# Kernel optimization log

Measured on AMD Instinct MI355X. Metric: run time of the kernel, lower is better.

Reference implementation:

```python
import jax, jax.numpy as jnp
import numpy as np
import math

B, S, E = 16, 600, 300   # batch, seq_len, enc_len
H, NC = 512, 2           # hidden, classes
D = S * E                # archi[0] = 180000


def setup_inputs() -> dict:
    key = jax.random.key(0)
    ks = jax.random.split(key, 7)
    x = jax.random.normal(ks[0], (B, S, E), dtype=jnp.float32)
    y = jax.random.randint(ks[1], (B,), 0, NC)
    # neurons initialized to zeros (init_neurons)
    n0 = jnp.zeros((B, S, E), jnp.float32)
    n1 = jnp.zeros((B, H), jnp.float32)
    n2 = jnp.zeros((B, NC), jnp.float32)
    # Linear weights (torch layout: [out, in]), Kaiming-uniform-like scale 1/sqrt(fan_in)
    W0 = jax.random.uniform(ks[2], (E, E), jnp.float32, -1.0, 1.0) / math.sqrt(E)
    W1 = jax.random.uniform(ks[3], (H, D), jnp.float32, -1.0, 1.0) / math.sqrt(D)
    b1 = jax.random.uniform(ks[4], (H,), jnp.float32, -1.0, 1.0) / math.sqrt(D)
    W2 = jax.random.uniform(ks[5], (NC, H), jnp.float32, -1.0, 1.0) / math.sqrt(H)
    b2 = jax.random.uniform(ks[6], (NC,), jnp.float32, -1.0, 1.0) / math.sqrt(H)
    return dict(x=x, y=y, n0=n0, n1=n1, n2=n2, W0=W0, W1=W1, b1=b1, W2=W2, b2=b2, T=3)


def reference(x, y, n0, n1, n2, W0, W1, b1, W2, b2, T):
    # EqProp free-phase relaxation (beta = 0.0, forward default).
    # Analytic dPhi/dneurons replaces torch.autograd.grad:
    scale = 1.0 / math.sqrt(E)
    Wx = jnp.einsum('bse,fe->bsf', x, W0)  # synapses[0](x), constant across steps
    for _ in range(T):
        g0 = Wx + (n1 @ W1).reshape(B, S, E)              # dPhi/dn0
        g1 = n0.reshape(B, D) @ W1.T + b1 + n2 @ W2       # dPhi/dn1
        g2 = n1 @ W2.T + b2                               # dPhi/dn2 (beta=0)
        # hand-coded attention update for neuron 0: Q=g0, K=V=x
        attn = jax.nn.softmax(scale * jnp.einsum('bse,bte->bst', g0, x), axis=-1)
        n0 = jnp.einsum('bst,bte->bse', attn, x)
        n1 = jnp.tanh(g1)
        n2 = jnp.tanh(g2)
    return n0, n1, n2
```

## Files before the change

kernel.cpp:

```cpp
#include <hip/hip_runtime.h>
#include <math.h>

#define DD 180000L
#define HH 512
#define BB 16
#define SS 600
#define EE 300
#define SP 608
#define EP 320

typedef unsigned short u16;
typedef __attribute__((ext_vector_type(8))) __bf16 bf16x8;
typedef __attribute__((ext_vector_type(4))) float f32x4;

__device__ __forceinline__ u16 f2bf(float f) {
  union { float f; unsigned int u; } x; x.f = f;
  unsigned int r = (x.u + 0x7FFFu + ((x.u >> 16) & 1u)) >> 16;
  return (u16)r;
}

__global__ __launch_bounds__(256) void k_conv_x(const float* __restrict__ x,
                                                u16* __restrict__ xb, u16* __restrict__ xt) {
  __shared__ u16 tl[32][33];
  int b = blockIdx.z;
  int tt = blockIdx.x * 32, ee = blockIdx.y * 32;
  int lx = threadIdx.x & 31, ly = threadIdx.x >> 5;
#pragma unroll
  for (int i = 0; i < 4; ++i) {
    int t = tt + ly + i * 8, e = ee + lx;
    float v = (t < SS && e < EE) ? x[((long)b * SS + t) * EE + e] : 0.f;
    u16 h = f2bf(v);
    xb[((long)b * SP + t) * EP + e] = h;
    tl[ly + i * 8][lx] = h;
  }
  __syncthreads();
#pragma unroll
  for (int i = 0; i < 4; ++i) {
    int e = ee + ly + i * 8, t = tt + lx;
    xt[((long)b * EP + e) * SP + t] = tl[lx][ly + i * 8];
  }
}

__global__ __launch_bounds__(256) void k_conv_w0(const float* __restrict__ W0, u16* __restrict__ w0b) {
  int idx = blockIdx.x * 256 + threadIdx.x;
  int f = idx / EP, e = idx % EP;
  float v = (f < EE && e < EE) ? W0[f * EE + e] : 0.f;
  w0b[idx] = f2bf(v);
}

__global__ __launch_bounds__(256) void k_gemm_nt(
    const u16* __restrict__ A, int lda, long sA, int Arows,
    const u16* __restrict__ B, int ldb, long sB, int Brows,
    float* __restrict__ C, int ldc, long sC, int Mv, int Nv, int K,
    u16* __restrict__ Cb, int ldcb, long sCb) {
  int bz = blockIdx.z;
  int m0 = blockIdx.x * 64, n0 = blockIdx.y * 64;
  int lane = threadIdx.x & 63, wv = threadIdx.x >> 6;
  int wm = m0 + (wv >> 1) * 32, wn = n0 + (wv & 1) * 32;
  int q = lane >> 4, ln = lane & 15;
  const u16* Ab = A + (long)bz * sA;
  const u16* Bb = B + (long)bz * sB;
  long arow0 = (long)min(wm + ln, Arows - 1) * lda;
  long arow1 = (long)min(wm + 16 + ln, Arows - 1) * lda;
  long brow0 = (long)min(wn + ln, Brows - 1) * ldb;
  long brow1 = (long)min(wn + 16 + ln, Brows - 1) * ldb;
  f32x4 acc00 = {0.f,0.f,0.f,0.f}, acc01 = acc00, acc10 = acc00, acc11 = acc00;
  int ksteps = (K + 31) >> 5;
  for (int kk = 0; kk < ksteps; ++kk) {
    int k0 = kk * 32 + q * 8;
    bf16x8 a0 = *(const bf16x8*)(Ab + arow0 + k0);
    bf16x8 a1 = *(const bf16x8*)(Ab + arow1 + k0);
    bf16x8 b0 = *(const bf16x8*)(Bb + brow0 + k0);
    bf16x8 bv1 = *(const bf16x8*)(Bb + brow1 + k0);
    acc00 = __builtin_amdgcn_mfma_f32_16x16x32_bf16(a0, b0,  acc00, 0, 0, 0);
    acc01 = __builtin_amdgcn_mfma_f32_16x16x32_bf16(a0, bv1, acc01, 0, 0, 0);
    acc10 = __builtin_amdgcn_mfma_f32_16x16x32_bf16(a1, b0,  acc10, 0, 0, 0);
    acc11 = __builtin_amdgcn_mfma_f32_16x16x32_bf16(a1, bv1, acc11, 0, 0, 0);
  }
  float* Cp = C + (long)bz * sC;
  u16* Cbp = Cb ? (Cb + (long)bz * sCb) : (u16*)0;
#pragma unroll
  for (int sm = 0; sm < 2; ++sm) {
#pragma unroll
    for (int sn = 0; sn < 2; ++sn) {
      f32x4 acc = (sm == 0) ? ((sn == 0) ? acc00 : acc01) : ((sn == 0) ? acc10 : acc11);
#pragma unroll
      for (int r = 0; r < 4; ++r) {
        int m = wm + sm * 16 + q * 4 + r;
        int n = wn + sn * 16 + ln;
        if (m < Mv && n < Nv) {
          float v = acc[r];
          Cp[(long)m * ldc + n] = v;
          if (Cbp) Cbp[(long)m * ldcb + n] = f2bf(v);
        }
      }
    }
  }
}

#define BN 256
#define BK 64
#define NCH 704

__global__ __launch_bounds__(256) void k_fused_w1(
    const float* __restrict__ W1, const float* __restrict__ n1f,
    const float* __restrict__ n0f, const float* __restrict__ Wx,
    u16* __restrict__ g0b, float* __restrict__ part) {
  __shared__ u16 wt[BK][BN + 8];
  __shared__ u16 n1s[BB][HH + 8];
  __shared__ u16 n0s[BB][BN + 8];
  int tid = threadIdx.x;
  long d0 = (long)blockIdx.x * BN;
#pragma unroll
  for (int i = 0; i < 8; ++i) {
    int f = i * 256 + tid;
    int b = f >> 7, c = (f & 127) * 4;
    float4 v = *(const float4*)(n1f + b * HH + c);
    n1s[b][c] = f2bf(v.x); n1s[b][c + 1] = f2bf(v.y);
    n1s[b][c + 2] = f2bf(v.z); n1s[b][c + 3] = f2bf(v.w);
  }
#pragma unroll
  for (int i = 0; i < 4; ++i) {
    int f = i * 256 + tid;
    int b = f >> 6, c = (f & 63) * 4;
    long d = d0 + c;
    float4 v = {0.f,0.f,0.f,0.f};
    if (d < DD) v = *(const float4*)(n0f + (long)b * DD + d);
    n0s[b][c] = f2bf(v.x); n0s[b][c + 1] = f2bf(v.y);
    n0s[b][c + 2] = f2bf(v.z); n0s[b][c + 3] = f2bf(v.w);
  }
  int lane = tid & 63, wv = tid >> 6, q = lane >> 4, ln = lane & 15;
  f32x4 acc0[4] = {{0.f,0.f,0.f,0.f},{0.f,0.f,0.f,0.f},{0.f,0.f,0.f,0.f},{0.f,0.f,0.f,0.f}};
  for (int s = 0; s < 8; ++s) {
    int h0 = s * BK;
    __syncthreads();
#pragma unroll
    for (int i = 0; i < 16; ++i) {
      int f = i * 256 + tid;
      int r = f >> 6, c = (f & 63) * 4;
      long d = d0 + c;
      float4 v = {0.f,0.f,0.f,0.f};
      if (d < DD) v = *(const float4*)(W1 + (long)(h0 + r) * DD + d);
      wt[r][c] = f2bf(v.x); wt[r][c + 1] = f2bf(v.y);
      wt[r][c + 2] = f2bf(v.z); wt[r][c + 3] = f2bf(v.w);
    }
    __syncthreads();
#pragma unroll
    for (int kst = 0; kst < 2; ++kst) {
      bf16x8 af = *(const bf16x8*)(&n1s[ln][h0 + kst * 32 + q * 8]);
#pragma unroll
      for (int nt = 0; nt < 4; ++nt) {
        int dc = wv * 64 + nt * 16 + ln;
        bf16x8 bv;
#pragma unroll
        for (int j = 0; j < 8; ++j) bv[j] = *(const __bf16*)(&wt[kst * 32 + q * 8 + j][dc]);
        acc0[nt] = __builtin_amdgcn_mfma_f32_16x16x32_bf16(af, bv, acc0[nt], 0, 0, 0);
      }
    }
    f32x4 acc1 = {0.f,0.f,0.f,0.f};
#pragma unroll
    for (int kst = 0; kst < 8; ++kst) {
      bf16x8 af = *(const bf16x8*)(&n0s[ln][kst * 32 + q * 8]);
      bf16x8 bv = *(const bf16x8*)(&wt[wv * 16 + ln][kst * 32 + q * 8]);
      acc1 = __builtin_amdgcn_mfma_f32_16x16x32_bf16(af, bv, acc1, 0, 0, 0);
    }
    long pb = (long)blockIdx.x * 8192;
#pragma unroll
    for (int r = 0; r < 4; ++r) {
      int b = q * 4 + r, h = h0 + wv * 16 + ln;
      part[pb + b * HH + h] = acc1[r];
    }
  }
#pragma unroll
  for (int nt = 0; nt < 4; ++nt) {
#pragma unroll
    for (int r = 0; r < 4; ++r) {
      int b = q * 4 + r;
      long d = d0 + wv * 64 + nt * 16 + ln;
      if (d < DD) {
        float val = Wx[(long)b * DD + d] + acc0[nt][r];
        int sI = (int)(d / EE), e = (int)(d % EE);
        g0b[((long)b * SS + sI) * EP + e] = f2bf(val);
      }
    }
  }
}

__global__ __launch_bounds__(256) void k_softmax(const float* __restrict__ S,
                                                 u16* __restrict__ P, float scale) {
  int s = blockIdx.x, b = blockIdx.y;
  const float* row = S + ((long)b * SP + s) * SP;
  u16* prow = P + ((long)b * SP + s) * SP;
  int tid = threadIdx.x, lane = tid & 63, wv = tid >> 6;
  __shared__ float red[8];
  float v[3]; float mx = -1e30f;
#pragma unroll
  for (int i = 0; i < 3; ++i) {
    int c = tid + i * 256;
    v[i] = (c < SS) ? row[c] * scale : -1e30f;
    mx = fmaxf(mx, v[i]);
  }
  for (int off = 32; off; off >>= 1) mx = fmaxf(mx, __shfl_down(mx, off));
  if (lane == 0) red[wv] = mx;
  __syncthreads();
  mx = fmaxf(fmaxf(red[0], red[1]), fmaxf(red[2], red[3]));
  float e[3], sum = 0.f;
#pragma unroll
  for (int i = 0; i < 3; ++i) {
    int c = tid + i * 256;
    e[i] = (c < SS) ? __expf(v[i] - mx) : 0.f;
    sum += e[i];
  }
  for (int off = 32; off; off >>= 1) sum += __shfl_down(sum, off);
  if (lane == 0) red[4 + wv] = sum;
  __syncthreads();
  float inv = 1.f / (red[4] + red[5] + red[6] + red[7]);
#pragma unroll
  for (int i = 0; i < 3; ++i) {
    int c = tid + i * 256;
    if (c < SS) prow[c] = f2bf(e[i] * inv);
  }
}

__global__ __launch_bounds__(256) void k_init(const float* __restrict__ b1, const float* __restrict__ b2,
                                              float* __restrict__ n1, float* __restrict__ n2) {
  int idx = blockIdx.x * 256 + threadIdx.x;
  n1[idx] = tanhf(b1[idx & 511]);
  if (idx < 32) n2[idx] = tanhf(b2[idx & 1]);
}

__global__ __launch_bounds__(64) void k_g2(const float* __restrict__ n1old, const float* __restrict__ W2,
                                           const float* __restrict__ b2, float* __restrict__ n2out) {
  int b = blockIdx.x >> 1, c = blockIdx.x & 1, lane = threadIdx.x;
  float s = 0.f;
#pragma unroll
  for (int i = 0; i < 8; ++i) { int h = lane + i * 64; s += n1old[b * HH + h] * W2[c * HH + h]; }
  for (int off = 32; off; off >>= 1) s += __shfl_down(s, off);
  if (lane == 0) n2out[b * 2 + c] = tanhf(s + b2[c]);
}

__global__ __launch_bounds__(256) void k_reduce1(const float* __restrict__ part, float* __restrict__ part2) {
  int idx = blockIdx.x * 256 + threadIdx.x;
  int sl = blockIdx.y;
  float s = 0.f;
  int c0 = sl * 88;
#pragma unroll 4
  for (int c = 0; c < 88; ++c) s += part[(long)(c0 + c) * 8192 + idx];
  part2[(long)sl * 8192 + idx] = s;
}

__global__ __launch_bounds__(256) void k_reduce2(const float* __restrict__ part2, const float* __restrict__ b1,
                                                 const float* __restrict__ W2, const float* __restrict__ n2old,
                                                 float* __restrict__ n1out) {
  int idx = blockIdx.x * 256 + threadIdx.x;
  int b = idx >> 9, h = idx & 511;
  float s = b1[h] + n2old[b * 2] * W2[h] + n2old[b * 2 + 1] * W2[HH + h];
#pragma unroll
  for (int sl = 0; sl < 8; ++sl) s += part2[(long)sl * 8192 + idx];
  n1out[idx] = tanhf(s);
}

extern "C" void kernel_launch(void* const* d_in, const int* in_sizes, int n_in,
                              void* d_out, int out_size, void* d_ws, size_t ws_size,
                              hipStream_t stream) {
  const float* x  = (const float*)d_in[0];
  const float* W0 = (const float*)d_in[5];
  const float* W1 = (const float*)d_in[6];
  const float* b1 = (const float*)d_in[7];
  const float* W2 = (const float*)d_in[8];
  const float* b2 = (const float*)d_in[9];

  float* out_n0 = (float*)d_out;
  float* out_n1 = out_n0 + 16L * SS * EE;
  float* out_n2 = out_n1 + 16L * HH;

  char* w = (char*)d_ws;
  auto take = [&](size_t bytes) { char* p = w; w += (bytes + 255) & ~(size_t)255; return p; };
  u16*   xb    = (u16*)take(16L * SP * EP * 2);
  u16*   xt    = (u16*)take(16L * EP * SP * 2);
  u16*   w0b   = (u16*)take((size_t)EP * EP * 2);
  float* Wx    = (float*)take(16L * SS * EE * 4);
  u16*   g0b   = (u16*)take(16L * SS * EP * 2);
  float* Sb    = (float*)take(16L * SP * SP * 4);
  u16*   attn  = (u16*)take(16L * SP * SP * 2);
  float* part2 = (float*)take(8L * 8192 * 4);
  float* n1A   = (float*)take(8192 * 4);
  float* n1B   = (float*)take(8192 * 4);
  float* n2A   = (float*)take(256);
  float* n2B   = (float*)take(256);
  float* part  = Sb;

  const float scale = 1.0f / sqrtf((float)EE);

  k_conv_x<<<dim3(19, 10, 16), 256, 0, stream>>>(x, xb, xt);
  k_conv_w0<<<400, 256, 0, stream>>>(W0, w0b);
  k_gemm_nt<<<dim3(10, 5, 16), 256, 0, stream>>>(xb, EP, (long)SP * EP, SP,
                                                 w0b, EP, 0, EP,
                                                 Wx, EE, (long)SS * EE, SS, EE, EE,
                                                 g0b, EP, (long)SS * EP);
  k_init<<<32, 256, 0, stream>>>(b1, b2, n1A, n2A);

  for (int it = 0; it < 3; ++it) {
    if (it > 0) {
      const float* n1old = (it == 1) ? n1A : n1B;
      const float* n2old = (it == 1) ? n2A : n2B;
      float* n2new = (it == 1) ? n2B : out_n2;
      float* n1new = (it == 1) ? n1B : out_n1;
      k_g2<<<32, 64, 0, stream>>>(n1old, W2, b2, n2new);
      k_fused_w1<<<NCH, 256, 0, stream>>>(W1, n1old, out_n0, Wx, g0b, part);
      k_reduce1<<<dim3(32, 8), 256, 0, stream>>>(part, part2);
      k_reduce2<<<32, 256, 0, stream>>>(part2, b1, W2, n2old, n1new);
    }
    k_gemm_nt<<<dim3(10, 10, 16), 256, 0, stream>>>(g0b, EP, (long)SS * EP, SS,
                                                    xb, EP, (long)SP * EP, SP,
                                                    Sb, SP, (long)SP * SP, SP, SP, EE,
                                                    (u16*)0, 0, 0);
    k_softmax<<<dim3(SS, 16), 256, 0, stream>>>(Sb, attn, scale);
    k_gemm_nt<<<dim3(10, 5, 16), 256, 0, stream>>>(attn, SP, (long)SP * SP, SP,
                                                   xt, SP, (long)EP * SP, EP,
                                                   out_n0, EE, (long)DD, SS, EE, SP,
                                                   (u16*)0, 0, 0);
  }
}
```

Before: 971.7 us.

## Fuse QK^T, softmax and PV into single flash-style attention kernel

Replaces the three-kernel attention path (score GEMM to fp32 buffer, softmax to bf16 buffer, PV GEMM) with one kernel per 16-row query tile. Each single-wave block holds the whole score row in registers, does the softmax in place, stages P in swizzled LDS, and multiplies by V^T directly. This removes the round trips through the large score and probability buffers and two launches. In exchange it uses very many registers per wave (38 score tiles plus 19 accumulators), runs only 608 one-wave blocks, and re-reads K and V from global memory in every block with no LDS sharing, which may limit occupancy and bandwidth. The part buffer is now allocated separately instead of aliasing the removed score buffer.

```diff
diff --git a/kernel.cpp b/kernel.cpp
--- a/kernel.cpp
+++ b/kernel.cpp
@@ -186,39 +186,105 @@
   }
 }
 
-__global__ __launch_bounds__(256) void k_softmax(const float* __restrict__ S,
-                                                 u16* __restrict__ P, float scale) {
-  int s = blockIdx.x, b = blockIdx.y;
-  const float* row = S + ((long)b * SP + s) * SP;
-  u16* prow = P + ((long)b * SP + s) * SP;
-  int tid = threadIdx.x, lane = tid & 63, wv = tid >> 6;
-  __shared__ float red[8];
-  float v[3]; float mx = -1e30f;
-#pragma unroll
-  for (int i = 0; i < 3; ++i) {
-    int c = tid + i * 256;
-    v[i] = (c < SS) ? row[c] * scale : -1e30f;
-    mx = fmaxf(mx, v[i]);
-  }
-  for (int off = 32; off; off >>= 1) mx = fmaxf(mx, __shfl_down(mx, off));
-  if (lane == 0) red[wv] = mx;
-  __syncthreads();
-  mx = fmaxf(fmaxf(red[0], red[1]), fmaxf(red[2], red[3]));
-  float e[3], sum = 0.f;
-#pragma unroll
-  for (int i = 0; i < 3; ++i) {
-    int c = tid + i * 256;
-    e[i] = (c < SS) ? __expf(v[i] - mx) : 0.f;
-    sum += e[i];
-  }
-  for (int off = 32; off; off >>= 1) sum += __shfl_down(sum, off);
-  if (lane == 0) red[4 + wv] = sum;
-  __syncthreads();
-  float inv = 1.f / (red[4] + red[5] + red[6] + red[7]);
-#pragma unroll
-  for (int i = 0; i < 3; ++i) {
-    int c = tid + i * 256;
-    if (c < SS) prow[c] = f2bf(e[i] * inv);
+#define SWZB(r) ((((r) >> 1) & 7) << 4)
+
+__global__ __launch_bounds__(64, 2) void k_attn(
+    const u16* __restrict__ Qg, const u16* __restrict__ Kg,
+    const u16* __restrict__ Vtg, float* __restrict__ O, float scale) {
+  __shared__ u16 P[16 * SP];
+  int b = blockIdx.y, tile = blockIdx.x;
+  int lane = threadIdx.x;
+  int q = lane >> 4, ln = lane & 15, q4 = q * 4;
+  const u16* Qb = Qg + (long)b * SS * EP;
+  const u16* Kb = Kg + (long)b * SP * EP;
+  const u16* Vb = Vtg + (long)b * EP * SP;
+
+  int qrow = min(tile * 16 + ln, SS - 1);
+  bf16x8 qf[10];
+#pragma unroll
+  for (int kk = 0; kk < 10; ++kk)
+    qf[kk] = *(const bf16x8*)(Qb + (long)qrow * EP + kk * 32 + q * 8);
+
+  f32x4 s[38];
+#pragma unroll
+  for (int j = 0; j < 38; ++j) {
+    const u16* Kr = Kb + (long)(j * 16 + ln) * EP + q * 8;
+    f32x4 sa = {0.f, 0.f, 0.f, 0.f}, sb = {0.f, 0.f, 0.f, 0.f};
+#pragma unroll
+    for (int kk = 0; kk < 10; kk += 2) {
+      bf16x8 k0 = *(const bf16x8*)(Kr + kk * 32);
+      bf16x8 k1 = *(const bf16x8*)(Kr + kk * 32 + 32);
+      sa = __builtin_amdgcn_mfma_f32_16x16x32_bf16(qf[kk], k0, sa, 0, 0, 0);
+      sb = __builtin_amdgcn_mfma_f32_16x16x32_bf16(qf[kk + 1], k1, sb, 0, 0, 0);
+    }
+    s[j] = sa + sb;
+  }
+
+  float mx[4] = {-3e38f, -3e38f, -3e38f, -3e38f};
+#pragma unroll
+  for (int j = 0; j < 38; ++j) {
+    bool msk = (j == 37) && (ln >= 8);
+#pragma unroll
+    for (int r = 0; r < 4; ++r) {
+      float v = msk ? -3e38f : s[j][r];
+      mx[r] = fmaxf(mx[r], v);
+    }
+  }
+#pragma unroll
+  for (int off = 8; off; off >>= 1)
+#pragma unroll
+    for (int r = 0; r < 4; ++r) mx[r] = fmaxf(mx[r], __shfl_xor(mx[r], off));
+  float sm[4] = {0.f, 0.f, 0.f, 0.f};
+#pragma unroll
+  for (int j = 0; j < 38; ++j) {
+    bool msk = (j == 37) && (ln >= 8);
+#pragma unroll
+    for (int r = 0; r < 4; ++r) {
+      float e = msk ? 0.f : __expf(scale * (s[j][r] - mx[r]));
+      s[j][r] = e;
+      sm[r] += e;
+    }
+  }
+#pragma unroll
+  for (int off = 8; off; off >>= 1)
+#pragma unroll
+    for (int r = 0; r < 4; ++r) sm[r] += __shfl_xor(sm[r], off);
+#pragma unroll
+  for (int r = 0; r < 4; ++r) sm[r] = 1.f / sm[r];
+
+#pragma unroll
+  for (int j = 0; j < 38; ++j) {
+#pragma unroll
+    for (int r = 0; r < 4; ++r) {
+      int row = q4 + r, t = j * 16 + ln;
+      unsigned byt = (unsigned)row * 1216 + (unsigned)t * 2;
+      P[(byt ^ SWZB(row)) >> 1] = f2bf(s[j][r] * sm[r]);
+    }
+  }
+
+  f32x4 acc[19];
+#pragma unroll
+  for (int nt = 0; nt < 19; ++nt) acc[nt] = (f32x4){0.f, 0.f, 0.f, 0.f};
+#pragma unroll
+  for (int kt = 0; kt < 19; ++kt) {
+    unsigned byt = (unsigned)ln * 1216 + (unsigned)kt * 64 + (unsigned)q * 16;
+    bf16x8 pa = *(const bf16x8*)(&P[(byt ^ SWZB(ln)) >> 1]);
+#pragma unroll
+    for (int nt = 0; nt < 19; ++nt) {
+      bf16x8 bv = *(const bf16x8*)(Vb + (long)(nt * 16 + ln) * SP + kt * 32 + q * 8);
+      acc[nt] = __builtin_amdgcn_mfma_f32_16x16x32_bf16(pa, bv, acc[nt], 0, 0, 0);
+    }
+  }
+
+  float* Ob = O + (long)b * SS * EE;
+  int m0 = tile * 16 + q4;
+#pragma unroll
+  for (int nt = 0; nt < 19; ++nt) {
+#pragma unroll
+    for (int r = 0; r < 4; ++r) {
+      int m = m0 + r, n = nt * 16 + ln;
+      if (m < SS && n < EE) Ob[(long)m * EE + n] = acc[nt][r];
+    }
   }
 }
 
@@ -281,14 +347,12 @@
   u16*   w0b   = (u16*)take((size_t)EP * EP * 2);
   float* Wx    = (float*)take(16L * SS * EE * 4);
   u16*   g0b   = (u16*)take(16L * SS * EP * 2);
-  float* Sb    = (float*)take(16L * SP * SP * 4);
-  u16*   attn  = (u16*)take(16L * SP * SP * 2);
+  float* part  = (float*)take((size_t)NCH * 8192 * 4);
   float* part2 = (float*)take(8L * 8192 * 4);
   float* n1A   = (float*)take(8192 * 4);
   float* n1B   = (float*)take(8192 * 4);
   float* n2A   = (float*)take(256);
   float* n2B   = (float*)take(256);
-  float* part  = Sb;
 
   const float scale = 1.0f / sqrtf((float)EE);
 
@@ -311,14 +375,6 @@
       k_reduce1<<<dim3(32, 8), 256, 0, stream>>>(part, part2);
       k_reduce2<<<32, 256, 0, stream>>>(part2, b1, W2, n2old, n1new);
     }
-    k_gemm_nt<<<dim3(10, 10, 16), 256, 0, stream>>>(g0b, EP, (long)SS * EP, SS,
-                                                    xb, EP, (long)SP * EP, SP,
-                                                    Sb, SP, (long)SP * SP, SP, SP, EE,
-                                                    (u16*)0, 0, 0);
-    k_softmax<<<dim3(SS, 16), 256, 0, stream>>>(Sb, attn, scale);
-    k_gemm_nt<<<dim3(10, 5, 16), 256, 0, stream>>>(attn, SP, (long)SP * SP, SP,
-                                                   xt, SP, (long)EP * SP, EP,
-                                                   out_n0, EE, (long)DD, SS, EE, SP,
-                                                   (u16*)0, 0, 0);
-  }
-}
+    k_attn<<<dim3(38, 16), 64, 0, stream>>>(g0b, xb, xt, out_n0, scale);
+  }
+}
```

Measured after the change: 1.065 ms. +9.6%, slower.
